# Kernel optimization log

Measured on AMD Instinct MI355X. Metric: run time of the kernel, lower is better.

Reference implementation:

```python
import jax, jax.numpy as jnp
import numpy as np

N_NODES = 100000
N_EDGES = 1600000
D_IN = 128
D_HID = 128
D_OUT = 2
BN_EPS = 1e-5


def _sage_conv(x, src, dst, W_l, b_l, W_r):
    # PyG SAGEConv (aggr='mean'): out = lin_l(mean_{j in N(i)} x_j) + lin_r(x_i)
    # messages flow src -> dst
    agg = jax.ops.segment_sum(x[src], dst, num_segments=x.shape[0])
    deg = jax.ops.segment_sum(jnp.ones((src.shape[0],), x.dtype), dst,
                              num_segments=x.shape[0])
    mean = agg / jnp.maximum(deg, 1.0)[:, None]
    return mean @ W_l + b_l + x @ W_r


def _batch_norm(x, gamma, beta):
    # training-mode BatchNorm1d math over the node dimension (biased var)
    mu = jnp.mean(x, axis=0)
    var = jnp.var(x, axis=0)
    return (x - mu) * jax.lax.rsqrt(var + BN_EPS) * gamma + beta


def setup_inputs() -> dict:
    key = jax.random.key(0)
    ks = jax.random.split(key, 10)
    s = lambda d: 1.0 / np.sqrt(d)
    x = jax.random.normal(ks[0], (N_NODES, D_IN), dtype=jnp.float32)
    edge_index = jax.random.randint(ks[1], (2, N_EDGES), 0, N_NODES, dtype=jnp.int64)
    W1l = jax.random.uniform(ks[2], (D_IN, D_HID), jnp.float32, -s(D_IN), s(D_IN))
    b1 = jax.random.uniform(ks[3], (D_HID,), jnp.float32, -s(D_IN), s(D_IN))
    W1r = jax.random.uniform(ks[4], (D_IN, D_HID), jnp.float32, -s(D_IN), s(D_IN))
    W2l = jax.random.uniform(ks[5], (D_HID, D_OUT), jnp.float32, -s(D_HID), s(D_HID))
    b2 = jax.random.uniform(ks[6], (D_OUT,), jnp.float32, -s(D_HID), s(D_HID))
    W2r = jax.random.uniform(ks[7], (D_HID, D_OUT), jnp.float32, -s(D_HID), s(D_HID))
    gamma1 = jnp.ones((D_HID,), jnp.float32)
    beta1 = jnp.zeros((D_HID,), jnp.float32)
    gamma2 = jnp.ones((D_OUT,), jnp.float32)
    beta2 = jnp.zeros((D_OUT,), jnp.float32)
    return {"x": x, "edge_index": edge_index,
            "W1l": W1l, "b1": b1, "W1r": W1r, "gamma1": gamma1, "beta1": beta1,
            "W2l": W2l, "b2": b2, "W2r": W2r, "gamma2": gamma2, "beta2": beta2}


def reference(x, edge_index, W1l, b1, W1r, gamma1, beta1,
              W2l, b2, W2r, gamma2, beta2):
    src, dst = edge_index[0], edge_index[1]
    h = _sage_conv(x, src, dst, W1l, b1, W1r)
    h = _batch_norm(h, gamma1, beta1)
    h = jax.nn.relu(h)
    # dropout in eval mode = identity
    h = _sage_conv(h, src, dst, W2l, b2, W2r)
    h = _batch_norm(h, gamma2, beta2)
    return jax.nn.log_softmax(h, axis=1)
```

## Files before the change

### kernel.cpp

```cpp
#include <hip/hip_runtime.h>
#include <hip/hip_bf16.h>
#include <math.h>


#define DH 128
#define PAD 64
#define NPB 128
#define CAPB (NPB * PAD)
#define MAXBINS 1024
#define MAXCHUNK 6400
#define SENT 0xFFFFFFFFu
#define L1BLOCKS 512

typedef short short8 __attribute__((ext_vector_type(8)));
typedef float float4v __attribute__((ext_vector_type(4)));
typedef float float2v __attribute__((ext_vector_type(2)));
typedef unsigned uint4v __attribute__((ext_vector_type(4)));

template <typename T> static __device__ __forceinline__ float tof(T v);
template <> __device__ __forceinline__ float tof<float>(float v) { return v; }
template <> __device__ __forceinline__ float tof<__hip_bfloat16>(__hip_bfloat16 v) {
  return __bfloat162float(v);
}

static __device__ __forceinline__ short f2bf_s(float f) {
  union { __hip_bfloat16 h; short s; } u;
  u.h = __float2bfloat16(f);
  return u.s;
}

static __device__ __forceinline__ float bf2f(short s) {
  union { unsigned u; float f; } c;
  c.u = ((unsigned)(unsigned short)s) << 16;
  return c.f;
}

static __device__ __forceinline__ float asf(unsigned u) {
  union { unsigned u; float f; } c;
  c.u = u;
  return c.f;
}

__global__ void k_probe(const unsigned* __restrict__ xw,
                        const unsigned* __restrict__ ew,
                        int* __restrict__ flags) {
  int t = threadIdx.x;
  unsigned wx = xw[(size_t)t * 23456 + 7];
  unsigned el = (wx >> 7) & 0xFFu;
  int sx = (el >= 0x60 && el <= 0x85) ? 1 : 0;
  unsigned we = ew[(size_t)t * 12000 + 1];
  int se = (we == 0) ? 1 : 0;
  __shared__ int c[2];
  if (t < 2) c[t] = 0;
  __syncthreads();
  atomicAdd(&c[0], sx);
  atomicAdd(&c[1], se);
  __syncthreads();
  if (t == 0) {
    flags[0] = (c[0] < 192) ? 1 : 0;
    flags[2] = (c[1] > 192) ? 1 : 0;
  }
}

template <typename FT>
static __device__ __forceinline__ void wt_one(const FT* __restrict__ W1l,
                                              const FT* __restrict__ W1r,
                                              short* __restrict__ WT, int idx) {
  int n = idx >> 8, k = idx & 255;
  float v = (k < 128) ? tof(W1l[k * 128 + n]) : tof(W1r[(k - 128) * 128 + n]);
  WT[n * 256 + k] = f2bf_s(v);
}
__global__ void k_xbwt(const void* __restrict__ x, const void* __restrict__ W1l,
                       const void* __restrict__ W1r, const int* __restrict__ flags,
                       __hip_bfloat162* __restrict__ xb, short* __restrict__ WT,
                       int total2) {
  int gi = blockIdx.x * blockDim.x + threadIdx.x;
  bool f32 = flags[0] != 0;
  if (gi < 32768) {
    if (f32) wt_one<float>((const float*)W1l, (const float*)W1r, WT, gi);
    else wt_one<__hip_bfloat16>((const __hip_bfloat16*)W1l, (const __hip_bfloat16*)W1r, WT, gi);
  }
  int i = gi - 32768;
  if (i >= 0 && i < total2) {
    if (f32) {
      float2 v = ((const float2*)x)[i];
      __hip_bfloat162 o;
      o.x = __float2bfloat16(v.x);
      o.y = __float2bfloat16(v.y);
      xb[i] = o;
    } else {
      xb[i] = ((const __hip_bfloat162*)x)[i];
    }
  }
}

template <typename IT>
static __device__ __forceinline__ void binscatter_agg_body(
    const IT* __restrict__ es, const IT* __restrict__ ed,
    int* __restrict__ binCnt, unsigned* __restrict__ pairs,
    int E, int N, int chunk, int NB) {
  __shared__ int cnt[MAXBINS];
  __shared__ int sc[MAXBINS];
  __shared__ int gbase[MAXBINS];
  __shared__ unsigned buf[MAXCHUNK];
  int t = threadIdx.x;
  int e0 = blockIdx.x * chunk;
  int e1 = min(e0 + chunk, E);
  int nE = e1 - e0;

  for (int b = t; b < MAXBINS; b += 256) cnt[b] = 0;
  __syncthreads();
  for (int i = t; i < nE; i += 256) {
    int d = (int)ed[e0 + i];
    if ((unsigned)d >= (unsigned)N) d = 0;
    atomicAdd(&cnt[d >> 7], 1);
  }
  __syncthreads();
  for (int b = t; b < MAXBINS; b += 256) sc[b] = cnt[b];
  __syncthreads();
  for (int off = 1; off < MAXBINS; off <<= 1) {
    int v[MAXBINS / 256];
#pragma unroll
    for (int j = 0; j < MAXBINS / 256; ++j) {
      int b = t + j * 256;
      v[j] = (b >= off) ? sc[b - off] : 0;
    }
    __syncthreads();
#pragma unroll
    for (int j = 0; j < MAXBINS / 256; ++j) sc[t + j * 256] += v[j];
    __syncthreads();
  }
  for (int b = t; b < NB; b += 256) {
    int c = cnt[b];
    sc[b] -= c;
    int g = 0;
    if (c > 0) g = atomicAdd(&binCnt[b * 16], (c + 15) & ~15);
    gbase[b] = g;
    cnt[b] = 0;
  }
  __syncthreads();
  for (int i = t; i < nE; i += 256) {
    int s = (int)es[e0 + i], d = (int)ed[e0 + i];
    if ((unsigned)s >= (unsigned)N) s = 0;
    if ((unsigned)d >= (unsigned)N) d = 0;
    int bin = d >> 7;
    int p = atomicAdd(&cnt[bin], 1);
    buf[sc[bin] + p] = ((unsigned)(d & (NPB - 1)) << 20) | (unsigned)s;
  }
  __syncthreads();
  for (int b = t; b < NB; b += 256) {
    int c = cnt[b];
    if (c == 0) continue;
    int g = gbase[b];
    if (g >= CAPB) continue;
    int cpad = (c + 15) & ~15;
    if (g + cpad > CAPB) cpad = CAPB - g;
    int cv = min(c, cpad);
    unsigned* dst = pairs + (size_t)b * CAPB + g;
    const unsigned* srcp = buf + sc[b];
    int j = 0;
    for (; j < cv; ++j) dst[j] = srcp[j];
    for (; j < cpad; ++j) dst[j] = SENT;
  }
}
__launch_bounds__(256)
__global__ void k_binscatter_agg(const void* __restrict__ ev, const int* __restrict__ flags,
                                 int* __restrict__ binCnt, unsigned* __restrict__ pairs,
                                 int E, int N, int chunk, int NB) {
  if (flags[2]) binscatter_agg_body<long long>((const long long*)ev, (const long long*)ev + E,
                                               binCnt, pairs, E, N, chunk, NB);
  else          binscatter_agg_body<int>((const int*)ev, (const int*)ev + E,
                                         binCnt, pairs, E, N, chunk, NB);
}

__launch_bounds__(256)
__global__ void k_binbuild(const unsigned* __restrict__ pairs,
                           const int* __restrict__ binCnt,
                           int* __restrict__ deg_i, int* __restrict__ srcs_pad, int N) {
  __shared__ int cnt[NPB];
  __shared__ int lst[NPB * PAD];
  int bin = blockIdx.x;
  int t = threadIdx.x;
  for (int i = t; i < NPB; i += 256) cnt[i] = 0;
  __syncthreads();
  int m = min(binCnt[bin * 16], CAPB);
  const unsigned* pp = pairs + (size_t)bin * CAPB;
  for (int i = t; i < m; i += 256) {
    unsigned u = pp[i];
    if (u == SENT) continue;
    int local = u >> 20;
    int s = u & 0xFFFFF;
    int r = atomicAdd(&cnt[local], 1);
    if (r < PAD) lst[local * PAD + r] = s;
  }
  __syncthreads();
  int base = bin * NPB;
  for (int i = t; i < NPB; i += 256) {
    int node = base + i;
    if (node < N) deg_i[node] = cnt[i];
  }
  for (int i = t; i < NPB * PAD; i += 256) {
    int node = base + (i >> 6);
    if (node < N) srcs_pad[(size_t)base * PAD + i] = lst[i];
  }
}

static __device__ __forceinline__ void accum8(float2v acc[4], uint4v u) {
#pragma unroll
  for (int i = 0; i < 4; ++i) {
    float2v p;
    p[0] = asf(u[i] << 16);
    p[1] = asf(u[i] & 0xFFFF0000u);
    acc[i] += p;
  }
}
__launch_bounds__(256)
__global__ void k_gather(const unsigned* __restrict__ xbu,
                         const int* __restrict__ deg_i, const int* __restrict__ srcs_pad,
                         short* __restrict__ meanbs, int N) {
  int node = blockIdx.x * 4 + (threadIdx.x >> 6);
  int lane = threadIdx.x & 63;
  int g = lane >> 4, l = lane & 15;
  if (node >= N) return;
  int dg = deg_i[node];
  int cnt = min(dg, PAD);
  const int* sl = srcs_pad + (size_t)node * PAD;
  const uint4v* xv = (const uint4v*)xbu;
  float2v acc[4];
#pragma unroll
  for (int i = 0; i < 4; ++i) acc[i] = (float2v){0.f, 0.f};

  int j = 0;
  for (; j + 16 <= cnt; j += 16) {
    uint4v v0 = xv[(size_t)sl[j + g]      * 16 + l];
    uint4v v1 = xv[(size_t)sl[j + 4 + g]  * 16 + l];
    uint4v v2 = xv[(size_t)sl[j + 8 + g]  * 16 + l];
    uint4v v3 = xv[(size_t)sl[j + 12 + g] * 16 + l];
    accum8(acc, v0);
    accum8(acc, v1);
    accum8(acc, v2);
    accum8(acc, v3);
  }
  for (; j + 8 <= cnt; j += 8) {
    uint4v va = xv[(size_t)sl[j + g] * 16 + l];
    uint4v vb = xv[(size_t)sl[j + 4 + g] * 16 + l];
    accum8(acc, va);
    accum8(acc, vb);
  }
  for (; j + 4 <= cnt; j += 4) {
    uint4v v = xv[(size_t)sl[j + g] * 16 + l];
    accum8(acc, v);
  }
  if (j + g < cnt) {
    uint4v v = xv[(size_t)sl[j + g] * 16 + l];
    accum8(acc, v);
  }

#pragma unroll
  for (int i = 0; i < 4; ++i) {
#pragma unroll
    for (int c = 0; c < 2; ++c) {
      acc[i][c] += __shfl_xor(acc[i][c], 16);
      acc[i][c] += __shfl_xor(acc[i][c], 32);
    }
  }
  if (g == 0) {
    float invd = 1.0f / fmaxf((float)dg, 1.0f);
    short8 o;
#pragma unroll
    for (int i = 0; i < 4; ++i) {
      o[2 * i]     = f2bf_s(acc[i][0] * invd);
      o[2 * i + 1] = f2bf_s(acc[i][1] * invd);
    }
    *(short8*)(meanbs + (size_t)node * DH + l * 8) = o;
  }
}

template <typename FT>
static __device__ __forceinline__ void layer1_body(
    const short* __restrict__ meanbs, const short* __restrict__ xbs,
    const short* __restrict__ WTs, const FT* __restrict__ b1,
    __hip_bfloat16* __restrict__ h1, float* __restrict__ partial,
    int N, int ntiles) {
  int w = threadIdx.x >> 6;
  int lane = threadIdx.x & 63;
  int m = lane & 15;
  int quad = lane >> 4;

  float bs[8], bq[8];
#pragma unroll
  for (int c = 0; c < 8; ++c) { bs[c] = 0.f; bq[c] = 0.f; }
  float bias[8];
#pragma unroll
  for (int c = 0; c < 8; ++c) bias[c] = tof(b1[c * 16 + m]);

  for (int tt = blockIdx.x; tt < ntiles; tt += gridDim.x) {
    int rowbase = tt * 64 + w * 16;
    int arowc = min(rowbase + m, N - 1);

    short8 afrag[8];
    const short* mr = meanbs + (size_t)arowc * DH;
#pragma unroll
    for (int kt = 0; kt < 4; ++kt)
      afrag[kt] = *(const short8*)(mr + kt * 32 + quad * 8);
    const short* xr = xbs + (size_t)arowc * DH;
#pragma unroll
    for (int kt = 0; kt < 4; ++kt)
      afrag[4 + kt] = *(const short8*)(xr + kt * 32 + quad * 8);

    float4v acc[8];
#pragma unroll
    for (int c = 0; c < 8; ++c) acc[c] = (float4v){0.f, 0.f, 0.f, 0.f};

#pragma unroll
    for (int kt = 0; kt < 8; ++kt) {
#pragma unroll
      for (int c = 0; c < 8; ++c) {
        short8 b = *(const short8*)(WTs + (c * 16 + m) * 256 + kt * 32 + quad * 8);
        acc[c] = __builtin_amdgcn_mfma_f32_16x16x32_bf16(afrag[kt], b, acc[c], 0, 0, 0);
      }
    }

#pragma unroll
    for (int c = 0; c < 8; ++c) {
      int col = c * 16 + m;
#pragma unroll
      for (int r = 0; r < 4; ++r) {
        int ro = rowbase + quad * 4 + r;
        float v = acc[c][r] + bias[c];
        if (ro < N) {
          h1[(size_t)ro * DH + col] = __float2bfloat16(v);
          bs[c] += v;
          bq[c] += v * v;
        }
      }
    }
  }

  __shared__ float lsum[4][128];
  __shared__ float lsq[4][128];
#pragma unroll
  for (int c = 0; c < 8; ++c) {
    float s = bs[c], q = bq[c];
    s += __shfl_xor(s, 16); s += __shfl_xor(s, 32);
    q += __shfl_xor(q, 16); q += __shfl_xor(q, 32);
    if (quad == 0) { lsum[w][c * 16 + m] = s; lsq[w][c * 16 + m] = q; }
  }
  __syncthreads();
  int t = threadIdx.x;
  if (t < 128) {
    float s = lsum[0][t] + lsum[1][t] + lsum[2][t] + lsum[3][t];
    float q = lsq[0][t] + lsq[1][t] + lsq[2][t] + lsq[3][t];
    partial[(size_t)blockIdx.x * 256 + t] = s;
    partial[(size_t)blockIdx.x * 256 + 128 + t] = q;
  }
}
__launch_bounds__(256)
__global__ void k_layer1(const short* __restrict__ meanbs, const short* __restrict__ xbs,
                         const short* __restrict__ WTs, const void* __restrict__ b1,
                         const int* __restrict__ flags,
                         __hip_bfloat16* __restrict__ h1, float* __restrict__ partial,
                         int N, int ntiles) {
  if (flags[0])
    layer1_body<float>(meanbs, xbs, WTs, (const float*)b1, h1, partial, N, ntiles);
  else
    layer1_body<__hip_bfloat16>(meanbs, xbs, WTs, (const __hip_bfloat16*)b1,
                                h1, partial, N, ntiles);
}

__global__ void k_stats1(const float* __restrict__ partial, float* __restrict__ st1,
                         int nblocks) {
  int c = threadIdx.x;
  float s = 0.f;
  for (int b = blockIdx.x; b < nblocks; b += gridDim.x)
    s += partial[(size_t)b * 256 + c];
  unsafeAtomicAdd(&st1[c], s);
}

template <typename FT>
static __device__ __forceinline__ void zr_body(
    const short* __restrict__ h1s, const float* __restrict__ stats1,
    const FT* __restrict__ g1, const FT* __restrict__ be1,
    const FT* __restrict__ W2l, const FT* __restrict__ W2r,
    float4* __restrict__ zr, int N) {
  __shared__ float sc[128], sh[128];
  int t = threadIdx.x;
  if (t < 128) {
    float invN = 1.0f / (float)N;
    float mu = stats1[t] * invN;
    float var = stats1[128 + t] * invN - mu * mu;
    float a = tof(g1[t]) * rsqrtf(var + 1e-5f);
    sc[t] = a;
    sh[t] = tof(be1[t]) - mu * a;
  }
  __syncthreads();
  int lane = t & 63, w = t >> 6;
  int g = lane >> 4, l = lane & 15;
  int f0 = l * 8;
  float scl[8], shl[8], wl0[8], wl1[8], wr0[8], wr1[8];
#pragma unroll
  for (int j = 0; j < 8; ++j) {
    int f = f0 + j;
    scl[j] = sc[f];
    shl[j] = sh[f];
    wl0[j] = tof(W2l[f * 2 + 0]);
    wl1[j] = tof(W2l[f * 2 + 1]);
    wr0[j] = tof(W2r[f * 2 + 0]);
    wr1[j] = tof(W2r[f * 2 + 1]);
  }
  int gw = blockIdx.x * 4 + w;
  int nw = gridDim.x * 4;
  for (int base = gw * 4; base < N; base += nw * 4) {
    int node = base + g;
    if (node < N) {
      short8 hv = *(const short8*)(h1s + (size_t)node * DH + f0);
      float z0 = 0.f, z1 = 0.f, r0 = 0.f, r1 = 0.f;
#pragma unroll
      for (int j = 0; j < 8; ++j) {
        float v = fmaxf(bf2f(hv[j]) * scl[j] + shl[j], 0.0f);
        z0 += v * wl0[j];
        z1 += v * wl1[j];
        r0 += v * wr0[j];
        r1 += v * wr1[j];
      }
#pragma unroll
      for (int off = 8; off >= 1; off >>= 1) {
        z0 += __shfl_xor(z0, off);
        z1 += __shfl_xor(z1, off);
        r0 += __shfl_xor(r0, off);
        r1 += __shfl_xor(r1, off);
      }
      if (l == 0) zr[node] = make_float4(z0, z1, r0, r1);
    }
  }
}
__launch_bounds__(256)
__global__ void k_zr(const __hip_bfloat16* __restrict__ h1, const float* __restrict__ st1,
                     const void* g1, const void* be1, const void* W2l, const void* W2r,
                     const int* __restrict__ flags, float4* __restrict__ zr, int N) {
  if (flags[0])
    zr_body<float>((const short*)h1, st1, (const float*)g1, (const float*)be1,
                   (const float*)W2l, (const float*)W2r, zr, N);
  else
    zr_body<__hip_bfloat16>((const short*)h1, st1, (const __hip_bfloat16*)g1,
                            (const __hip_bfloat16*)be1,
                            (const __hip_bfloat16*)W2l, (const __hip_bfloat16*)W2r, zr, N);
}

template <typename FT>
static __device__ __forceinline__ void h2_body(
    const float2* __restrict__ z2, const int* __restrict__ deg_i,
    const int* __restrict__ srcs_pad, const FT* __restrict__ b2,
    float2* __restrict__ h2, float* __restrict__ stats2, int N) {
  int lane = threadIdx.x & 63, w = threadIdx.x >> 6;
  int g = lane >> 4, l = lane & 15;
  float bs0 = 0.f, bs1 = 0.f, bq0 = 0.f, bq1 = 0.f;
  float bb0 = tof(b2[0]), bb1 = tof(b2[1]);
  int gw = blockIdx.x * 4 + w;
  int nw = gridDim.x * 4;
  for (int base = gw * 4; base < N; base += nw * 4) {
    int node = base + g;
    float za = 0.f, zb = 0.f;
    int dg_true = 0;
    if (node < N) {
      dg_true = deg_i[node];
      int cnt = min(dg_true, PAD);
      const int* sl = srcs_pad + (size_t)node * PAD;
      for (int j = l; j < cnt; j += 16) {
        float2 v = z2[2 * sl[j]];
        za += v.x;
        zb += v.y;
      }
    }
#pragma unroll
    for (int off = 8; off >= 1; off >>= 1) {
      za += __shfl_xor(za, off);
      zb += __shfl_xor(zb, off);
    }
    if (node < N && l == 0) {
      float dg = fmaxf((float)dg_true, 1.0f);
      float2 rw = z2[2 * node + 1];
      float h0 = za / dg + rw.x + bb0;
      float h1v = zb / dg + rw.y + bb1;
      h2[node] = make_float2(h0, h1v);
      bs0 += h0; bs1 += h1v; bq0 += h0 * h0; bq1 += h1v * h1v;
    }
  }
  bs0 += __shfl_xor(bs0, 16); bs0 += __shfl_xor(bs0, 32);
  bs1 += __shfl_xor(bs1, 16); bs1 += __shfl_xor(bs1, 32);
  bq0 += __shfl_xor(bq0, 16); bq0 += __shfl_xor(bq0, 32);
  bq1 += __shfl_xor(bq1, 16); bq1 += __shfl_xor(bq1, 32);
  __shared__ float red[4][4];
  if (lane == 0) { red[w][0] = bs0; red[w][1] = bs1; red[w][2] = bq0; red[w][3] = bq1; }
  __syncthreads();
  if (threadIdx.x < 4) {
    float a = red[0][threadIdx.x] + red[1][threadIdx.x] +
              red[2][threadIdx.x] + red[3][threadIdx.x];
    unsafeAtomicAdd(&stats2[threadIdx.x], a);
  }
}
__launch_bounds__(256)
__global__ void k_h2(const float4* __restrict__ zr, const int* __restrict__ deg_i,
                     const int* __restrict__ srcs_pad, const void* b2,
                     const int* __restrict__ flags,
                     float2* __restrict__ h2, float* __restrict__ stats2, int N) {
  if (flags[0])
    h2_body<float>((const float2*)zr, deg_i, srcs_pad, (const float*)b2, h2, stats2, N);
  else
    h2_body<__hip_bfloat16>((const float2*)zr, deg_i, srcs_pad,
                            (const __hip_bfloat16*)b2, h2, stats2, N);
}

template <typename FT>
static __device__ __forceinline__ void out_body(
    const float2* __restrict__ h2, const float* __restrict__ stats2,
    const FT* __restrict__ g2, const FT* __restrict__ be2,
    void* __restrict__ out, int N) {
  int i = blockIdx.x * blockDim.x + threadIdx.x;
  if (i >= N) return;
  float invN = 1.0f / (float)N;
  float mu0 = stats2[0] * invN, mu1 = stats2[1] * invN;
  float v0 = stats2[2] * invN - mu0 * mu0;
  float v1 = stats2[3] * invN - mu1 * mu1;
  float r0 = rsqrtf(v0 + 1e-5f), r1 = rsqrtf(v1 + 1e-5f);
  float2 h = h2[i];
  float y0 = (h.x - mu0) * r0 * tof(g2[0]) + tof(be2[0]);
  float y1 = (h.y - mu1) * r1 * tof(g2[1]) + tof(be2[1]);
  float mx = fmaxf(y0, y1);
  float lse = mx + logf(expf(y0 - mx) + expf(y1 - mx));
  float o0 = y0 - lse, o1 = y1 - lse;
  if (sizeof(FT) == 4) {
    ((float2*)out)[i] = make_float2(o0, o1);
  } else {
    __hip_bfloat162 o;
    o.x = __float2bfloat16(o0);
    o.y = __float2bfloat16(o1);
    ((__hip_bfloat162*)out)[i] = o;
  }
}
__global__ void k_out(const float2* __restrict__ h2, const float* __restrict__ stats2,
                      const void* g2, const void* be2, const int* __restrict__ flags,
                      void* __restrict__ out, int N) {
  if (flags[0]) out_body<float>(h2, stats2, (const float*)g2, (const float*)be2, out, N);
  else out_body<__hip_bfloat16>(h2, stats2, (const __hip_bfloat16*)g2,
                                (const __hip_bfloat16*)be2, out, N);
}

extern "C" void kernel_launch(void* const* d_in, const int* in_sizes, int n_in,
                              void* d_out, int out_size, void* d_ws, size_t ws_size,
                              hipStream_t stream) {
  int ix = 0, ie = 1, iW1l = 2, ib1 = 3, iW1r = 4, ig1 = 5, ibe1 = 6,
      iW2l = 7, ib2 = 8, iW2r = 9, ig2 = 10, ibe2 = 11;
  if (n_in == 12) {
    int best = -1, second = -1;
    for (int i = 0; i < 12; ++i) {
      if (best < 0 || in_sizes[i] > in_sizes[best]) { second = best; best = i; }
      else if (second < 0 || in_sizes[i] > in_sizes[second]) second = i;
    }
    ix = best; ie = second;
    int c16384 = 0, c128 = 0, c256 = 0, c2 = 0;
    for (int i = 0; i < 12; ++i) {
      if (i == ix || i == ie) continue;
      int s = in_sizes[i];
      if (s == 16384) { if (c16384++ == 0) iW1l = i; else iW1r = i; }
      else if (s == 128) { if (c128 == 0) ib1 = i; else if (c128 == 1) ig1 = i; else ibe1 = i; c128++; }
      else if (s == 256) { if (c256++ == 0) iW2l = i; else iW2r = i; }
      else { if (c2 == 0) ib2 = i; else if (c2 == 1) ig2 = i; else ibe2 = i; c2++; }
    }
  }

  const void* x   = d_in[ix];
  const void* ev  = d_in[ie];
  const void* W1l = d_in[iW1l];
  const void* b1  = d_in[ib1];
  const void* W1r = d_in[iW1r];
  const void* g1  = d_in[ig1];
  const void* be1 = d_in[ibe1];
  const void* W2l = d_in[iW2l];
  const void* b2  = d_in[ib2];
  const void* W2r = d_in[iW2r];
  const void* g2  = d_in[ig2];
  const void* be2 = d_in[ibe2];

  int N = in_sizes[ix] / DH;
  int E = in_sizes[ie] / 2;
  int nb = (N + 63) / 64;
  int NB = (N + NPB - 1) / NPB;

  int nblk = (E + MAXCHUNK - 1) / MAXCHUNK;
  if (nblk < 256) nblk = 256;
  int chunk = (E + nblk - 1) / nblk;

  int grid1 = (nb < L1BLOCKS) ? nb : L1BLOCKS;

  char* ws = (char*)d_ws;
  size_t off = 0;
  auto alloc = [&](size_t b) { size_t o = off; off += (b + 255) & ~(size_t)255; return o; };
  size_t o_st1   = alloc(256 * 4);
  size_t o_st2   = alloc(4 * 4);
  size_t o_bcnt  = alloc((size_t)NB * 16 * 4);
  size_t zlen = off;
  size_t o_pairs = alloc((size_t)NB * CAPB * 4);
  size_t o_degi  = alloc((size_t)N * 4);
  size_t o_srcs  = alloc((size_t)N * PAD * 4);
  size_t o_xb    = alloc((size_t)N * DH * 2);
  size_t o_mean  = alloc((size_t)N * DH * 2);
  size_t o_h1    = alloc((size_t)N * DH * 2);
  size_t o_wt    = alloc(256 * 128 * 2);
  size_t o_zr    = alloc((size_t)N * 16);
  size_t o_h2    = alloc((size_t)N * 8);
  size_t o_part  = alloc((size_t)L1BLOCKS * 256 * 4);
  size_t o_flg   = alloc(64);

  float* st1  = (float*)(ws + o_st1);
  float* st2  = (float*)(ws + o_st2);
  int* bcnt   = (int*)(ws + o_bcnt);
  unsigned* pairs = (unsigned*)(ws + o_pairs);
  int* deg_i  = (int*)(ws + o_degi);
  int* srcs   = (int*)(ws + o_srcs);
  __hip_bfloat162* xb = (__hip_bfloat162*)(ws + o_xb);
  short* meanb = (short*)(ws + o_mean);
  __hip_bfloat16* h1 = (__hip_bfloat16*)(ws + o_h1);
  short* WT   = (short*)(ws + o_wt);
  float4* zrp = (float4*)(ws + o_zr);
  float2* h2p = (float2*)(ws + o_h2);
  float* part = (float*)(ws + o_part);
  int* flags  = (int*)(ws + o_flg);

  hipMemsetAsync(d_ws, 0, zlen, stream);

  int total2 = N * 64;
  k_probe<<<1, 256, 0, stream>>>((const unsigned*)x, (const unsigned*)ev, flags);
  k_xbwt<<<(total2 + 32768 + 255) / 256, 256, 0, stream>>>(x, W1l, W1r, flags, xb, WT, total2);
  k_binscatter_agg<<<nblk, 256, 0, stream>>>(ev, flags, bcnt, pairs, E, N, chunk, NB);
  k_binbuild<<<NB, 256, 0, stream>>>(pairs, bcnt, deg_i, srcs, N);
  k_gather<<<(N + 3) / 4, 256, 0, stream>>>((const unsigned*)xb, deg_i, srcs, meanb, N);
  k_layer1<<<grid1, 256, 0, stream>>>(meanb, (const short*)xb, WT, b1,
                                      flags, h1, part, N, nb);
  k_stats1<<<64, 256, 0, stream>>>(part, st1, grid1);
  k_zr<<<512, 256, 0, stream>>>(h1, st1, g1, be1, W2l, W2r, flags, zrp, N);
  k_h2<<<2048, 256, 0, stream>>>(zrp, deg_i, srcs, b2, flags, h2p, st2, N);
  k_out<<<(N + 255) / 256, 256, 0, stream>>>(h2p, st2, g2, be2, flags, d_out, N);
}
```

Before: 330.0 us.

## Drop pair padding, prefetch gather indices via shuffles, fuse BN stats atomics

Several changes at once. The binscatter kernel no longer pads each bin segment to a multiple of 16 with sentinels, and binbuild zero-initialises its shared list instead. The gather kernel loads all 64 source indices per node with one coalesced load, broadcasts them with shuffles, and issues up to 32 row loads up front with masking in place of tail loops. Layer1 now atomically accumulates BN statistics directly into st1, which removes the partial buffer and the k_stats1 launch. It also launches one block per tile, and grid sizes for binscatter and zr change. Together these aim to cut launch count, memory traffic and latency-bound loops, at the cost of more global atomics and wasted loads on masked lanes.

Result: slower. 381.0 us (+15.4%).

```diff
diff --git a/kernel.cpp b/kernel.cpp
--- a/kernel.cpp
+++ b/kernel.cpp
@@ -10,7 +10,6 @@
 #define MAXBINS 1024
 #define MAXCHUNK 6400
 #define SENT 0xFFFFFFFFu
-#define L1BLOCKS 512
 
 typedef short short8 __attribute__((ext_vector_type(8)));
 typedef float float4v __attribute__((ext_vector_type(4)));
@@ -107,6 +106,7 @@
   int e0 = blockIdx.x * chunk;
   int e1 = min(e0 + chunk, E);
   int nE = e1 - e0;
+  if (nE <= 0) return;
 
   for (int b = t; b < MAXBINS; b += 256) cnt[b] = 0;
   __syncthreads();
@@ -134,7 +134,7 @@
     int c = cnt[b];
     sc[b] -= c;
     int g = 0;
-    if (c > 0) g = atomicAdd(&binCnt[b * 16], (c + 15) & ~15);
+    if (c > 0) g = atomicAdd(&binCnt[b * 16], c);
     gbase[b] = g;
     cnt[b] = 0;
   }
@@ -153,14 +153,10 @@
     if (c == 0) continue;
     int g = gbase[b];
     if (g >= CAPB) continue;
-    int cpad = (c + 15) & ~15;
-    if (g + cpad > CAPB) cpad = CAPB - g;
-    int cv = min(c, cpad);
+    int cv = min(c, CAPB - g);
     unsigned* dst = pairs + (size_t)b * CAPB + g;
     const unsigned* srcp = buf + sc[b];
-    int j = 0;
-    for (; j < cv; ++j) dst[j] = srcp[j];
-    for (; j < cpad; ++j) dst[j] = SENT;
+    for (int j = 0; j < cv; ++j) dst[j] = srcp[j];
   }
 }
 __launch_bounds__(256)
@@ -182,6 +178,7 @@
   int bin = blockIdx.x;
   int t = threadIdx.x;
   for (int i = t; i < NPB; i += 256) cnt[i] = 0;
+  for (int i = t; i < NPB * PAD; i += 256) lst[i] = 0;
   __syncthreads();
   int m = min(binCnt[bin * 16], CAPB);
   const unsigned* pp = pairs + (size_t)bin * CAPB;
@@ -213,6 +210,13 @@
     p[1] = asf(u[i] & 0xFFFF0000u);
     acc[i] += p;
   }
+}
+static __device__ __forceinline__ uint4v maskv(uint4v v, int keep) {
+  unsigned m = keep ? 0xFFFFFFFFu : 0u;
+  uint4v r;
+#pragma unroll
+  for (int i = 0; i < 4; ++i) r[i] = v[i] & m;
+  return r;
 }
 __launch_bounds__(256)
 __global__ void k_gather(const unsigned* __restrict__ xbu,
@@ -225,35 +229,69 @@
   int dg = deg_i[node];
   int cnt = min(dg, PAD);
   const int* sl = srcs_pad + (size_t)node * PAD;
+  int srcv = sl[lane];
   const uint4v* xv = (const uint4v*)xbu;
   float2v acc[4];
 #pragma unroll
   for (int i = 0; i < 4; ++i) acc[i] = (float2v){0.f, 0.f};
 
-  int j = 0;
-  for (; j + 16 <= cnt; j += 16) {
-    uint4v v0 = xv[(size_t)sl[j + g]      * 16 + l];
-    uint4v v1 = xv[(size_t)sl[j + 4 + g]  * 16 + l];
-    uint4v v2 = xv[(size_t)sl[j + 8 + g]  * 16 + l];
-    uint4v v3 = xv[(size_t)sl[j + 12 + g] * 16 + l];
-    accum8(acc, v0);
-    accum8(acc, v1);
-    accum8(acc, v2);
-    accum8(acc, v3);
-  }
-  for (; j + 8 <= cnt; j += 8) {
-    uint4v va = xv[(size_t)sl[j + g] * 16 + l];
-    uint4v vb = xv[(size_t)sl[j + 4 + g] * 16 + l];
-    accum8(acc, va);
-    accum8(acc, vb);
-  }
-  for (; j + 4 <= cnt; j += 4) {
-    uint4v v = xv[(size_t)sl[j + g] * 16 + l];
-    accum8(acc, v);
-  }
-  if (j + g < cnt) {
-    uint4v v = xv[(size_t)sl[j + g] * 16 + l];
-    accum8(acc, v);
+  if (cnt > 0) {
+    int sA0 = __shfl(srcv, g);
+    int sA1 = __shfl(srcv, 4 + g);
+    int sA2 = __shfl(srcv, 8 + g);
+    int sA3 = __shfl(srcv, 12 + g);
+    uint4v a0 = xv[(size_t)sA0 * 16 + l];
+    uint4v a1 = xv[(size_t)sA1 * 16 + l];
+    uint4v a2 = xv[(size_t)sA2 * 16 + l];
+    uint4v a3 = xv[(size_t)sA3 * 16 + l];
+    uint4v b0, b1, b2, b3;
+    bool hb = cnt > 16;
+    if (hb) {
+      int sB0 = __shfl(srcv, 16 + g);
+      int sB1 = __shfl(srcv, 20 + g);
+      int sB2 = __shfl(srcv, 24 + g);
+      int sB3 = __shfl(srcv, 28 + g);
+      b0 = xv[(size_t)sB0 * 16 + l];
+      b1 = xv[(size_t)sB1 * 16 + l];
+      b2 = xv[(size_t)sB2 * 16 + l];
+      b3 = xv[(size_t)sB3 * 16 + l];
+    }
+    a0 = maskv(a0, g < cnt);
+    a1 = maskv(a1, 4 + g < cnt);
+    a2 = maskv(a2, 8 + g < cnt);
+    a3 = maskv(a3, 12 + g < cnt);
+    accum8(acc, a0);
+    accum8(acc, a1);
+    accum8(acc, a2);
+    accum8(acc, a3);
+    if (hb) {
+      b0 = maskv(b0, 16 + g < cnt);
+      b1 = maskv(b1, 20 + g < cnt);
+      b2 = maskv(b2, 24 + g < cnt);
+      b3 = maskv(b3, 28 + g < cnt);
+      accum8(acc, b0);
+      accum8(acc, b1);
+      accum8(acc, b2);
+      accum8(acc, b3);
+    }
+    for (int j = 32; j < cnt; j += 16) {
+      int s0 = __shfl(srcv, j + g);
+      int s1 = __shfl(srcv, j + 4 + g);
+      int s2 = __shfl(srcv, j + 8 + g);
+      int s3 = __shfl(srcv, j + 12 + g);
+      uint4v v0 = xv[(size_t)s0 * 16 + l];
+      uint4v v1 = xv[(size_t)s1 * 16 + l];
+      uint4v v2 = xv[(size_t)s2 * 16 + l];
+      uint4v v3 = xv[(size_t)s3 * 16 + l];
+      v0 = maskv(v0, j + g < cnt);
+      v1 = maskv(v1, j + 4 + g < cnt);
+      v2 = maskv(v2, j + 8 + g < cnt);
+      v3 = maskv(v3, j + 12 + g < cnt);
+      accum8(acc, v0);
+      accum8(acc, v1);
+      accum8(acc, v2);
+      accum8(acc, v3);
+    }
   }
 
 #pragma unroll
@@ -280,7 +318,7 @@
 static __device__ __forceinline__ void layer1_body(
     const short* __restrict__ meanbs, const short* __restrict__ xbs,
     const short* __restrict__ WTs, const FT* __restrict__ b1,
-    __hip_bfloat16* __restrict__ h1, float* __restrict__ partial,
+    __hip_bfloat16* __restrict__ h1, float* __restrict__ st1,
     int N, int ntiles) {
   int w = threadIdx.x >> 6;
   int lane = threadIdx.x & 63;
@@ -351,30 +389,21 @@
   if (t < 128) {
     float s = lsum[0][t] + lsum[1][t] + lsum[2][t] + lsum[3][t];
     float q = lsq[0][t] + lsq[1][t] + lsq[2][t] + lsq[3][t];
-    partial[(size_t)blockIdx.x * 256 + t] = s;
-    partial[(size_t)blockIdx.x * 256 + 128 + t] = q;
+    unsafeAtomicAdd(&st1[t], s);
+    unsafeAtomicAdd(&st1[128 + t], q);
   }
 }
 __launch_bounds__(256)
 __global__ void k_layer1(const short* __restrict__ meanbs, const short* __restrict__ xbs,
                          const short* __restrict__ WTs, const void* __restrict__ b1,
                          const int* __restrict__ flags,
-                         __hip_bfloat16* __restrict__ h1, float* __restrict__ partial,
+                         __hip_bfloat16* __restrict__ h1, float* __restrict__ st1,
                          int N, int ntiles) {
   if (flags[0])
-    layer1_body<float>(meanbs, xbs, WTs, (const float*)b1, h1, partial, N, ntiles);
+    layer1_body<float>(meanbs, xbs, WTs, (const float*)b1, h1, st1, N, ntiles);
   else
     layer1_body<__hip_bfloat16>(meanbs, xbs, WTs, (const __hip_bfloat16*)b1,
-                                h1, partial, N, ntiles);
-}
-
-__global__ void k_stats1(const float* __restrict__ partial, float* __restrict__ st1,
-                         int nblocks) {
-  int c = threadIdx.x;
-  float s = 0.f;
-  for (int b = blockIdx.x; b < nblocks; b += gridDim.x)
-    s += partial[(size_t)b * 256 + c];
-  unsafeAtomicAdd(&st1[c], s);
+                                h1, st1, N, ntiles);
 }
 
 template <typename FT>
@@ -587,11 +616,9 @@
   int nb = (N + 63) / 64;
   int NB = (N + NPB - 1) / NPB;
 
-  int nblk = (E + MAXCHUNK - 1) / MAXCHUNK;
-  if (nblk < 256) nblk = 256;
+  int nblk = 1024;
+  if ((E + nblk - 1) / nblk > MAXCHUNK) nblk = (E + MAXCHUNK - 1) / MAXCHUNK;
   int chunk = (E + nblk - 1) / nblk;
-
-  int grid1 = (nb < L1BLOCKS) ? nb : L1BLOCKS;
 
   char* ws = (char*)d_ws;
   size_t off = 0;
@@ -609,7 +636,6 @@
   size_t o_wt    = alloc(256 * 128 * 2);
   size_t o_zr    = alloc((size_t)N * 16);
   size_t o_h2    = alloc((size_t)N * 8);
-  size_t o_part  = alloc((size_t)L1BLOCKS * 256 * 4);
   size_t o_flg   = alloc(64);
 
   float* st1  = (float*)(ws + o_st1);
@@ -624,7 +650,6 @@
   short* WT   = (short*)(ws + o_wt);
   float4* zrp = (float4*)(ws + o_zr);
   float2* h2p = (float2*)(ws + o_h2);
-  float* part = (float*)(ws + o_part);
   int* flags  = (int*)(ws + o_flg);
 
   hipMemsetAsync(d_ws, 0, zlen, stream);
@@ -635,10 +660,9 @@
   k_binscatter_agg<<<nblk, 256, 0, stream>>>(ev, flags, bcnt, pairs, E, N, chunk, NB);
   k_binbuild<<<NB, 256, 0, stream>>>(pairs, bcnt, deg_i, srcs, N);
   k_gather<<<(N + 3) / 4, 256, 0, stream>>>((const unsigned*)xb, deg_i, srcs, meanb, N);
-  k_layer1<<<grid1, 256, 0, stream>>>(meanb, (const short*)xb, WT, b1,
-                                      flags, h1, part, N, nb);
-  k_stats1<<<64, 256, 0, stream>>>(part, st1, grid1);
-  k_zr<<<512, 256, 0, stream>>>(h1, st1, g1, be1, W2l, W2r, flags, zrp, N);
+  k_layer1<<<nb, 256, 0, stream>>>(meanb, (const short*)xb, WT, b1,
+                                   flags, h1, st1, N, nb);
+  k_zr<<<2048, 256, 0, stream>>>(h1, st1, g1, be1, W2l, W2r, flags, zrp, N);
   k_h2<<<2048, 256, 0, stream>>>(zrp, deg_i, srcs, b2, flags, h2p, st2, N);
   k_out<<<(N + 255) / 256, 256, 0, stream>>>(h2p, st2, g2, be2, flags, d_out, N);
 }
```
